# Kernel tuning notes

Measured on AMD Instinct MI355X. Metric: run time of the kernel, lower is better.

## Reference

```python
import jax, jax.numpy as jnp
import numpy as np

B, T, H = 4, 4096, 2048
NUM_HEADS, HEAD_DIM = 16, 128


def setup_inputs() -> dict:
    key = jax.random.key(0)
    k1, k2, k3 = jax.random.split(key, 3)
    hidden = jax.random.normal(k1, (B, T, H), dtype=jnp.float32)
    # Linear(H -> 3H): store weight as [H, 3H] for x @ W
    w_qkv = jax.random.normal(k2, (H, 3 * H), dtype=jnp.float32) * (1.0 / np.sqrt(H))
    b_qkv = jax.random.normal(k3, (3 * H,), dtype=jnp.float32) * 0.02
    return {"hidden": hidden, "w_qkv": w_qkv, "b_qkv": b_qkv}


def _to_heads(x):
    # (B, T, H) -> (B, num_heads, T, head_dim)
    b, t, _ = x.shape
    return x.reshape(b, t, NUM_HEADS, HEAD_DIM).transpose(0, 2, 1, 3)


def reference(hidden, w_qkv, b_qkv):
    # fused QKV projection: (B,T,H) @ (H,3H) + (3H,)
    qkv = jnp.einsum('bth,hd->btd', hidden, w_qkv) + b_qkv
    q, k, v = jnp.split(qkv, 3, axis=-1)
    return _to_heads(q), _to_heads(k), _to_heads(v)
```

## Files before the change

### kernel.cpp

```cpp
#include <hip/hip_runtime.h>
#include <hip/hip_bf16.h>
#include <stdint.h>

#define M_DIM 16384
#define K_DIM 2048
#define N_DIM 6144
#define NT    32
#define NTILES 6

typedef __attribute__((ext_vector_type(8))) short bf16x8;
typedef __attribute__((ext_vector_type(8))) unsigned short u16x8;
typedef __attribute__((ext_vector_type(4))) float f32x4;

__device__ __forceinline__ unsigned short f2bf(float f) {
  unsigned int u = __float_as_uint(f);
  u += 0x7FFFu + ((u >> 16) & 1u);
  return (unsigned short)(u >> 16);
}

__device__ __forceinline__ void load_lds16(const void* g, void* l) {
  __builtin_amdgcn_global_load_lds((const __attribute__((address_space(1))) void*)g,
                                   (__attribute__((address_space(3))) void*)l, 16, 0, 0);
}

#define FENCE asm volatile("" ::: "memory")
#define BAR   do { FENCE; __builtin_amdgcn_s_barrier(); FENCE; } while (0)

__global__ __launch_bounds__(256) void cvt_fused(const float* __restrict__ hidden,
                                                 unsigned short* __restrict__ outh,
                                                 const float* __restrict__ w,
                                                 unsigned short* __restrict__ wt) {
  __shared__ float tile[64][69];
  const int bid = blockIdx.x;
  const int t = threadIdx.x;
  if (bid < 2048) {
    unsigned int base = bid * 256u + t;
    #pragma unroll
    for (int i = 0; i < 16; ++i) {
      unsigned int fi = i * 524288u + base;
      f32x4 v = __builtin_nontemporal_load(reinterpret_cast<const f32x4*>(hidden) + fi);
      ushort4 o;
      o.x = f2bf(v[0]); o.y = f2bf(v[1]); o.z = f2bf(v[2]); o.w = f2bf(v[3]);
      reinterpret_cast<ushort4*>(outh)[fi] = o;
    }
  } else {
    const int wb = bid - 2048;
    const int k0 = (wb / 96) * 64;
    const int n0 = (wb % 96) * 64;
    #pragma unroll
    for (int i = 0; i < 4; ++i) {
      int idx = i * 256 + t;
      int row = idx >> 4, c4 = idx & 15;
      f32x4 v = __builtin_nontemporal_load(reinterpret_cast<const f32x4*>(
          &w[(size_t)(k0 + row) * N_DIM + n0 + c4 * 4]));
      tile[row][c4 * 4 + 0] = v[0]; tile[row][c4 * 4 + 1] = v[1];
      tile[row][c4 * 4 + 2] = v[2]; tile[row][c4 * 4 + 3] = v[3];
    }
    __syncthreads();
    #pragma unroll
    for (int i = 0; i < 2; ++i) {
      int idx = i * 256 + t;
      int n = idx >> 3, k8 = idx & 7;
      u16x8 v;
      #pragma unroll
      for (int e = 0; e < 8; ++e) v[e] = f2bf(tile[k8 * 8 + e][n]);
      *reinterpret_cast<u16x8*>(&wt[(size_t)(n0 + n) * K_DIM + k0 + k8 * 8]) = v;
    }
  }
}

__global__ __launch_bounds__(512, 2) void gemm_qkv_8ph(const unsigned short* __restrict__ A,
                                                       const unsigned short* __restrict__ Bt,
                                                       const float* __restrict__ bias,
                                                       float* __restrict__ out) {
  extern __shared__ __align__(16) char smem[];
  const int tid = threadIdx.x, lane = tid & 63, wid = tid >> 6;
  const int wm = wid >> 2, wn = wid & 3;

  const int xcd = blockIdx.x & 7;
  const int lcl = blockIdx.x >> 3;

  const int srow  = tid >> 3;
  const int sslot = (tid & 7) ^ ((tid >> 3) & 7);
  const int r15 = lane & 15, q4 = lane >> 4, x7 = lane & 7;
  const int abase = (wm * 128 + r15) * 128;
  const int bbase = (wn * 64  + r15) * 128;
  const int sw0 = ((0 + q4) ^ x7) * 16;
  const int sw1 = ((4 + q4) ^ x7) * 16;

  #define STAGE_T(gsrc, ldsbase)                                              \
    { const unsigned short* _g = (gsrc); char* _l = (ldsbase);                \
      load_lds16(_g,                       _l +     wid * 1024);              \
      load_lds16(_g + (size_t)64  * K_DIM, _l + 8192  + wid * 1024);          \
      load_lds16(_g + (size_t)128 * K_DIM, _l + 16384 + wid * 1024);          \
      load_lds16(_g + (size_t)192 * K_DIM, _l + 24576 + wid * 1024); }

  #define STAGE_H2(gsrc, ldsbase, cA, cB)                                     \
    { const unsigned short* _g = (gsrc); char* _l = (ldsbase);                \
      load_lds16(_g + (size_t)((cA) * 64) * K_DIM, _l + (cA) * 8192 + wid * 1024); \
      load_lds16(_g + (size_t)((cB) * 64) * K_DIM, _l + (cB) * 8192 + wid * 1024); }

  #define TILE_MAP(jj, m0_, n0_, gA_, gB_)                                    \
    { const int bm_ = xcd * 8 + (lcl >> 2);                                   \
      const int bn_ = (jj) * 4 + (lcl & 3);                                   \
      m0_ = bm_ * 256; n0_ = bn_ * 256;                                       \
      gA_ = A  + (size_t)(m0_ + srow) * K_DIM + sslot * 8;                    \
      gB_ = Bt + (size_t)(n0_ + srow) * K_DIM + sslot * 8; }

  if (tid < 384) {
    const int jj = tid / 64;
    const int o  = (tid & 63) * 4;
    const int bn_ = jj * 4 + (lcl & 3);
    f32x4 bv = *reinterpret_cast<const f32x4*>(&bias[bn_ * 256 + o]);
    *reinterpret_cast<f32x4*>(smem + 131072 + jj * 1024 + o * 4) = bv;
  }

  int m0, n0, m0n, n0n;
  const unsigned short *gA, *gB, *gAn, *gBn;
  TILE_MAP(0, m0, n0, gA, gB);
  {
    char* A0 = smem;          char* B0 = smem + 32768;
    char* A1 = smem + 65536;  char* B1 = smem + 98304;
    STAGE_T(gB +  0, B0); STAGE_T(gA +  0, A0);
    STAGE_T(gB + 64, B1); STAGE_T(gA + 64, A1);
    asm volatile("s_waitcnt vmcnt(8)" ::: "memory");
    BAR;
  }

  for (int j = 0; j < NTILES; ++j) {
    const int jn = (j + 1 < NTILES) ? j + 1 : j;
    TILE_MAP(jn, m0n, n0n, gAn, gBn);

    f32x4 bq[2][2];
    {
      const char* bl = smem + 131072 + j * 1024;
      #pragma unroll
      for (int qn = 0; qn < 2; ++qn)
        #pragma unroll
        for (int ni = 0; ni < 2; ++ni)
          bq[qn][ni] = *reinterpret_cast<const f32x4*>(
              bl + (wn * 64 + qn * 32 + ni * 16 + q4 * 4) * 4);
    }
    f32x4 acc[2][2][4][2];
    #pragma unroll
    for (int qm = 0; qm < 2; ++qm)
      #pragma unroll
      for (int qn = 0; qn < 2; ++qn)
        #pragma unroll
        for (int mi = 0; mi < 4; ++mi)
          #pragma unroll
          for (int ni = 0; ni < 2; ++ni)
            acc[qm][qn][mi][ni] = bq[qn][ni];

    bf16x8 a[4][2], b0[2][2], b1[2][2];

    for (int t = 0; t < NT; ++t) {
      char* Ab = smem + (t & 1) * 65536;
      char* Bb = Ab + 32768;
      const bool st = (t + 2 < NT) || (j + 1 < NTILES);
      const unsigned short* sA = (t + 2 < NT) ? gA + (size_t)(t + 2) * 64
                                              : gAn + (size_t)(t + 2 - NT) * 64;
      const unsigned short* sB = (t + 2 < NT) ? gB + (size_t)(t + 2) * 64
                                              : gBn + (size_t)(t + 2 - NT) * 64;

      #pragma unroll
      for (int mi = 0; mi < 4; ++mi) {
        const char* p = Ab + abase + mi * (16 * 128);
        a[mi][0] = *(const bf16x8*)(p + sw0);
        a[mi][1] = *(const bf16x8*)(p + sw1);
      }
      #pragma unroll
      for (int ni = 0; ni < 2; ++ni) {
        const char* p = Bb + bbase + ni * (16 * 128);
        b0[ni][0] = *(const bf16x8*)(p + sw0);
        b0[ni][1] = *(const bf16x8*)(p + sw1);
      }
      BAR;
      __builtin_amdgcn_s_setprio(1);
      #pragma unroll
      for (int mi = 0; mi < 4; ++mi)
        #pragma unroll
        for (int ni = 0; ni < 2; ++ni) {
          acc[0][0][mi][ni] = __builtin_amdgcn_mfma_f32_16x16x32_bf16(b0[ni][0], a[mi][0], acc[0][0][mi][ni], 0, 0, 0);
          acc[0][0][mi][ni] = __builtin_amdgcn_mfma_f32_16x16x32_bf16(b0[ni][1], a[mi][1], acc[0][0][mi][ni], 0, 0, 0);
        }
      __builtin_amdgcn_s_setprio(0);
      BAR;

      #pragma unroll
      for (int ni = 0; ni < 2; ++ni) {
        const char* p = Bb + bbase + (32 + ni * 16) * 128;
        b1[ni][0] = *(const bf16x8*)(p + sw0);
        b1[ni][1] = *(const bf16x8*)(p + sw1);
      }
      if (st) STAGE_H2(sA, Ab, 0, 2);
      BAR;
      __builtin_amdgcn_s_setprio(1);
      #pragma unroll
      for (int mi = 0; mi < 4; ++mi)
        #pragma unroll
        for (int ni = 0; ni < 2; ++ni) {
          acc[0][1][mi][ni] = __builtin_amdgcn_mfma_f32_16x16x32_bf16(b1[ni][0], a[mi][0], acc[0][1][mi][ni], 0, 0, 0);
          acc[0][1][mi][ni] = __builtin_amdgcn_mfma_f32_16x16x32_bf16(b1[ni][1], a[mi][1], acc[0][1][mi][ni], 0, 0, 0);
        }
      __builtin_amdgcn_s_setprio(0);
      BAR;

      #pragma unroll
      for (int mi = 0; mi < 4; ++mi) {
        const char* p = Ab + abase + (64 + mi * 16) * 128;
        a[mi][0] = *(const bf16x8*)(p + sw0);
        a[mi][1] = *(const bf16x8*)(p + sw1);
      }
      if (st) STAGE_H2(sB, Bb, 0, 1);
      BAR;
      __builtin_amdgcn_s_setprio(1);
      #pragma unroll
      for (int mi = 0; mi < 4; ++mi)
        #pragma unroll
        for (int ni = 0; ni < 2; ++ni) {
          acc[1][0][mi][ni] = __builtin_amdgcn_mfma_f32_16x16x32_bf16(b0[ni][0], a[mi][0], acc[1][0][mi][ni], 0, 0, 0);
          acc[1][0][mi][ni] = __builtin_amdgcn_mfma_f32_16x16x32_bf16(b0[ni][1], a[mi][1], acc[1][0][mi][ni], 0, 0, 0);
        }
      __builtin_amdgcn_s_setprio(0);
      BAR;

      if (st) { STAGE_H2(sB, Bb, 2, 3); STAGE_H2(sA, Ab, 1, 3); }
      BAR;
      __builtin_amdgcn_s_setprio(1);
      #pragma unroll
      for (int mi = 0; mi < 4; ++mi)
        #pragma unroll
        for (int ni = 0; ni < 2; ++ni) {
          acc[1][1][mi][ni] = __builtin_amdgcn_mfma_f32_16x16x32_bf16(b1[ni][0], a[mi][0], acc[1][1][mi][ni], 0, 0, 0);
          acc[1][1][mi][ni] = __builtin_amdgcn_mfma_f32_16x16x32_bf16(b1[ni][1], a[mi][1], acc[1][1][mi][ni], 0, 0, 0);
        }
      __builtin_amdgcn_s_setprio(0);
      if (t == 0 && j != 0)  { asm volatile("s_waitcnt vmcnt(40)" ::: "memory"); }
      else if (st)           { asm volatile("s_waitcnt vmcnt(8)"  ::: "memory"); }
      else                   { asm volatile("s_waitcnt vmcnt(0)"  ::: "memory"); }
      BAR;
    }

    #pragma unroll
    for (int qm = 0; qm < 2; ++qm)
      #pragma unroll
      for (int mi = 0; mi < 4; ++mi) {
        const int m = m0 + wm * 128 + qm * 64 + mi * 16 + r15;
        const int bb_ = m >> 12, tt = m & 4095;
        float* orow = out + (size_t)bb_ * 8388608 + (size_t)tt * 128;
        #pragma unroll
        for (int qn = 0; qn < 2; ++qn)
          #pragma unroll
          for (int ni = 0; ni < 2; ++ni) {
            const int col = n0 + wn * 64 + qn * 32 + ni * 16 + q4 * 4;
            const int which = col >> 11, head = (col & 2047) >> 7, hd = col & 127;
            *reinterpret_cast<f32x4*>(orow + (size_t)which * 33554432 +
                                      (size_t)head * 524288 + hd) = acc[qm][qn][mi][ni];
          }
      }

    m0 = m0n; n0 = n0n; gA = gAn; gB = gBn;
  }
  #undef STAGE_T
  #undef STAGE_H2
  #undef TILE_MAP
}

__global__ __launch_bounds__(256) void naive_qkv(const float* __restrict__ h,
                                                 const float* __restrict__ w,
                                                 const float* __restrict__ bias,
                                                 float* __restrict__ out) {
  const int m = blockIdx.x;
  const int n = blockIdx.y * 256 + threadIdx.x;
  const float* hr = h + (size_t)m * K_DIM;
  float acc = bias[n];
  for (int k = 0; k < K_DIM; ++k) acc = fmaf(hr[k], w[(size_t)k * N_DIM + n], acc);
  const int which = n >> 11, head = (n & 2047) >> 7, hd = n & 127;
  const int bb = m >> 12, tt = m & 4095;
  out[(size_t)which * 33554432 + (size_t)bb * 8388608 + (size_t)head * 524288 +
      (size_t)tt * 128 + hd] = acc;
}

extern "C" void kernel_launch(void* const* d_in, const int* in_sizes, int n_in,
                              void* d_out, int out_size, void* d_ws, size_t ws_size,
                              hipStream_t stream) {
  const float* hidden = (const float*)d_in[0];
  const float* w_qkv  = (const float*)d_in[1];
  const float* b_qkv  = (const float*)d_in[2];
  float* out = (float*)d_out;

  const size_t needA = (size_t)M_DIM * K_DIM * 2;
  const size_t needB = (size_t)N_DIM * K_DIM * 2;
  if (ws_size >= needA + needB) {
    unsigned short* Abf = (unsigned short*)d_ws;
    unsigned short* Wt  = (unsigned short*)((char*)d_ws + needA);
    (void)hipFuncSetAttribute((const void*)gemm_qkv_8ph,
                              hipFuncAttributeMaxDynamicSharedMemorySize, 137216);
    cvt_fused<<<5120, 256, 0, stream>>>(hidden, Abf, w_qkv, Wt);
    gemm_qkv_8ph<<<256, 512, 137216, stream>>>(Abf, Wt, b_qkv, out);
  } else {
    naive_qkv<<<dim3(16384, 24), 256, 0, stream>>>(hidden, w_qkv, b_qkv, out);
  }
}
```

Baseline: 441.0 us.

## Restructure main loop into two MFMA phases with reshuffled async staging

Collapses the four barrier-separated MFMA quarters per k-step into two phases by loading both B halves up front. The global-to-LDS staging is redistributed: one quarter of the A tile for step t+1 is issued in the first phase and the rest of A and B for step t+2 in the second. The vmcnt waits are retuned to match. This halves the barriers per iteration to cut sync overhead, but raises register pressure and changes how early the prefetched data lands, which risks stalls or LDS hazards if the waits are off.

Result: no change. 434.9 us (median of 2 runs) (-1.4%).

```diff
diff --git a/kernel.cpp b/kernel.cpp
--- a/kernel.cpp
+++ b/kernel.cpp
@@ -122,8 +122,9 @@
     char* A0 = smem;          char* B0 = smem + 32768;
     char* A1 = smem + 65536;  char* B1 = smem + 98304;
     STAGE_T(gB +  0, B0); STAGE_T(gA +  0, A0);
-    STAGE_T(gB + 64, B1); STAGE_T(gA + 64, A1);
-    asm volatile("s_waitcnt vmcnt(8)" ::: "memory");
+    STAGE_H2(gB + 64, B1, 0, 1); STAGE_H2(gB + 64, B1, 2, 3);
+    STAGE_H2(gA + 64, A1, 0, 2);
+    asm volatile("s_waitcnt vmcnt(6)" ::: "memory");
     BAR;
   }
 
@@ -155,26 +156,33 @@
     bf16x8 a[4][2], b0[2][2], b1[2][2];
 
     for (int t = 0; t < NT; ++t) {
-      char* Ab = smem + (t & 1) * 65536;
-      char* Bb = Ab + 32768;
-      const bool st = (t + 2 < NT) || (j + 1 < NTILES);
-      const unsigned short* sA = (t + 2 < NT) ? gA + (size_t)(t + 2) * 64
-                                              : gAn + (size_t)(t + 2 - NT) * 64;
-      const unsigned short* sB = (t + 2 < NT) ? gB + (size_t)(t + 2) * 64
-                                              : gBn + (size_t)(t + 2 - NT) * 64;
-
+      char* Ab  = smem + (t & 1) * 65536;
+      char* Bb  = Ab + 32768;
+      char* Ab1 = smem + (((t + 1) & 1) * 65536);
+      const bool st1 = (t + 1 < NT) || (j + 1 < NTILES);
+      const bool st2 = (t + 2 < NT) || (j + 1 < NTILES);
+      const unsigned short* sA1 = (t + 1 < NT) ? gA + (size_t)(t + 1) * 64 : gAn;
+      const unsigned short* sA2 = (t + 2 < NT) ? gA + (size_t)(t + 2) * 64
+                                               : gAn + (size_t)(t + 2 - NT) * 64;
+      const unsigned short* sB2 = (t + 2 < NT) ? gB + (size_t)(t + 2) * 64
+                                               : gBn + (size_t)(t + 2 - NT) * 64;
+
+      #pragma unroll
+      for (int ni = 0; ni < 2; ++ni) {
+        const char* p0 = Bb + bbase + ni * (16 * 128);
+        b0[ni][0] = *(const bf16x8*)(p0 + sw0);
+        b0[ni][1] = *(const bf16x8*)(p0 + sw1);
+        const char* p1 = Bb + bbase + (32 + ni * 16) * 128;
+        b1[ni][0] = *(const bf16x8*)(p1 + sw0);
+        b1[ni][1] = *(const bf16x8*)(p1 + sw1);
+      }
       #pragma unroll
       for (int mi = 0; mi < 4; ++mi) {
         const char* p = Ab + abase + mi * (16 * 128);
         a[mi][0] = *(const bf16x8*)(p + sw0);
         a[mi][1] = *(const bf16x8*)(p + sw1);
       }
-      #pragma unroll
-      for (int ni = 0; ni < 2; ++ni) {
-        const char* p = Bb + bbase + ni * (16 * 128);
-        b0[ni][0] = *(const bf16x8*)(p + sw0);
-        b0[ni][1] = *(const bf16x8*)(p + sw1);
-      }
+      if (st1) STAGE_H2(sA1, Ab1, 1, 3);
       BAR;
       __builtin_amdgcn_s_setprio(1);
       #pragma unroll
@@ -183,23 +191,6 @@
         for (int ni = 0; ni < 2; ++ni) {
           acc[0][0][mi][ni] = __builtin_amdgcn_mfma_f32_16x16x32_bf16(b0[ni][0], a[mi][0], acc[0][0][mi][ni], 0, 0, 0);
           acc[0][0][mi][ni] = __builtin_amdgcn_mfma_f32_16x16x32_bf16(b0[ni][1], a[mi][1], acc[0][0][mi][ni], 0, 0, 0);
-        }
-      __builtin_amdgcn_s_setprio(0);
-      BAR;
-
-      #pragma unroll
-      for (int ni = 0; ni < 2; ++ni) {
-        const char* p = Bb + bbase + (32 + ni * 16) * 128;
-        b1[ni][0] = *(const bf16x8*)(p + sw0);
-        b1[ni][1] = *(const bf16x8*)(p + sw1);
-      }
-      if (st) STAGE_H2(sA, Ab, 0, 2);
-      BAR;
-      __builtin_amdgcn_s_setprio(1);
-      #pragma unroll
-      for (int mi = 0; mi < 4; ++mi)
-        #pragma unroll
-        for (int ni = 0; ni < 2; ++ni) {
           acc[0][1][mi][ni] = __builtin_amdgcn_mfma_f32_16x16x32_bf16(b1[ni][0], a[mi][0], acc[0][1][mi][ni], 0, 0, 0);
           acc[0][1][mi][ni] = __builtin_amdgcn_mfma_f32_16x16x32_bf16(b1[ni][1], a[mi][1], acc[0][1][mi][ni], 0, 0, 0);
         }
@@ -212,7 +203,11 @@
         a[mi][0] = *(const bf16x8*)(p + sw0);
         a[mi][1] = *(const bf16x8*)(p + sw1);
       }
-      if (st) STAGE_H2(sB, Bb, 0, 1);
+      if (st2) {
+        STAGE_H2(sB2, Bb, 0, 1);
+        STAGE_H2(sB2, Bb, 2, 3);
+        STAGE_H2(sA2, Ab, 0, 2);
+      }
       BAR;
       __builtin_amdgcn_s_setprio(1);
       #pragma unroll
@@ -221,24 +216,12 @@
         for (int ni = 0; ni < 2; ++ni) {
           acc[1][0][mi][ni] = __builtin_amdgcn_mfma_f32_16x16x32_bf16(b0[ni][0], a[mi][0], acc[1][0][mi][ni], 0, 0, 0);
           acc[1][0][mi][ni] = __builtin_amdgcn_mfma_f32_16x16x32_bf16(b0[ni][1], a[mi][1], acc[1][0][mi][ni], 0, 0, 0);
-        }
-      __builtin_amdgcn_s_setprio(0);
-      BAR;
-
-      if (st) { STAGE_H2(sB, Bb, 2, 3); STAGE_H2(sA, Ab, 1, 3); }
-      BAR;
-      __builtin_amdgcn_s_setprio(1);
-      #pragma unroll
-      for (int mi = 0; mi < 4; ++mi)
-        #pragma unroll
-        for (int ni = 0; ni < 2; ++ni) {
           acc[1][1][mi][ni] = __builtin_amdgcn_mfma_f32_16x16x32_bf16(b1[ni][0], a[mi][0], acc[1][1][mi][ni], 0, 0, 0);
           acc[1][1][mi][ni] = __builtin_amdgcn_mfma_f32_16x16x32_bf16(b1[ni][1], a[mi][1], acc[1][1][mi][ni], 0, 0, 0);
         }
       __builtin_amdgcn_s_setprio(0);
-      if (t == 0 && j != 0)  { asm volatile("s_waitcnt vmcnt(40)" ::: "memory"); }
-      else if (st)           { asm volatile("s_waitcnt vmcnt(8)"  ::: "memory"); }
-      else                   { asm volatile("s_waitcnt vmcnt(0)"  ::: "memory"); }
+      if (st2) { asm volatile("s_waitcnt vmcnt(6)" ::: "memory"); }
+      else     { asm volatile("s_waitcnt vmcnt(0)" ::: "memory"); }
       BAR;
     }
 
```
